# Performance work log

Measured on AMD Instinct MI355X. Metric: run time of the kernel, lower is better.

The kernel has to match this reference:

```python
import jax, jax.numpy as jnp
import numpy as np
from jax import lax

B, C, H, W = 8, 2, 1024, 1024
K = 500            # max_num
POST_MAX = 83      # circle_nms post_max_size
NMS_THRESH = 4.0   # squared-distance threshold in grid units
SCORE_THR = 0.1
# post_center_range converted to grid units per CenterPointBBoxCoder.__init__
PCR_LOW = jnp.array([-100.0, -100.0, -10.0], dtype=jnp.float32)
PCR_HIGH = jnp.array([1124.0, 1124.0, 10.0], dtype=jnp.float32)


def setup_inputs() -> dict:
    key = jax.random.key(0)
    ks = jax.random.split(key, 7)
    return {
        "heat": jax.random.uniform(ks[0], (B, C, H, W), dtype=jnp.float32),
        "reg": jax.random.normal(ks[1], (B, 2, H, W), dtype=jnp.float32),
        "rot_sine": jax.random.normal(ks[2], (B, 1, H, W), dtype=jnp.float32),
        "rot_cosine": jax.random.normal(ks[3], (B, 1, H, W), dtype=jnp.float32),
        "hei": jax.random.normal(ks[4], (B, 1, H, W), dtype=jnp.float32),
        "dim": jax.random.normal(ks[5], (B, 3, H, W), dtype=jnp.float32),
        "vel": jax.random.normal(ks[6], (B, 2, H, W), dtype=jnp.float32),
    }


def _gather_feat(feat_bnc, inds_bk):
    # feat: [B, N, Ch], inds: [B, K] -> [B, K, Ch]
    return jnp.take_along_axis(feat_bnc, inds_bk[:, :, None], axis=1)


def _transpose_and_gather(feat_bchw, inds_bk):
    # [B, Ch, H, W] -> gather at flat HW indices -> [B, K, Ch]
    b, c, h, w = feat_bchw.shape
    f = feat_bchw.transpose(0, 2, 3, 1).reshape(b, h * w, c)
    return _gather_feat(f, inds_bk)


def _topk(scores):
    # scores: [B, C, H, W]
    b, c, h, w = scores.shape
    topk_scores, topk_inds = lax.top_k(scores.reshape(b, c, h * w), K)  # [B,C,K]
    topk_inds = topk_inds % (h * w)
    topk_ys = (topk_inds // w).astype(jnp.float32)
    topk_xs = (topk_inds % w).astype(jnp.float32)
    topk_score, topk_ind = lax.top_k(topk_scores.reshape(b, c * K), K)  # [B,K]
    topk_clses = (topk_ind // K).astype(jnp.int32)
    gather2 = lambda t: jnp.take_along_axis(t.reshape(b, c * K), topk_ind, axis=1)
    return topk_score, gather2(topk_inds), topk_clses, gather2(topk_ys), gather2(topk_xs)


def _circle_nms_keep(x, y, s):
    # Sequential circle NMS per image (jit-compatible fori_loop).
    k = x.shape[0]
    order = jnp.argsort(-s)
    xs, ys = x[order], y[order]
    idx = jnp.arange(k)

    def body(i, supp):
        d2 = (xs - xs[i]) ** 2 + (ys - ys[i]) ** 2
        new = supp | ((idx > i) & (d2 <= NMS_THRESH))
        return jnp.where(supp[i], supp, new)

    supp = lax.fori_loop(0, k, body, jnp.zeros(k, dtype=bool))
    keep_sorted = ~supp
    keep_sorted = keep_sorted & (jnp.cumsum(keep_sorted.astype(jnp.int32)) <= POST_MAX)
    return jnp.zeros(k, dtype=bool).at[order].set(keep_sorted)


def reference(heat, reg, rot_sine, rot_cosine, hei, dim, vel):
    scores, inds, clses, ys, xs = _topk(heat)            # [B,K] each
    reg_g = _transpose_and_gather(reg, inds)             # [B,K,2]
    xs = xs[:, :, None] + reg_g[:, :, 0:1]
    ys = ys[:, :, None] + reg_g[:, :, 1:2]
    rot = jnp.arctan2(_transpose_and_gather(rot_sine, inds),
                      _transpose_and_gather(rot_cosine, inds))  # [B,K,1]
    hei_g = _transpose_and_gather(hei, inds)             # [B,K,1]
    dim_g = _transpose_and_gather(dim, inds)             # [B,K,3]
    vel_g = _transpose_and_gather(vel, inds)             # [B,K,2]
    boxes = jnp.concatenate([xs, ys, hei_g, dim_g, rot, vel_g], axis=2)  # [B,K,9]

    valid = (boxes[..., :3] >= PCR_LOW).all(-1) & (boxes[..., :3] <= PCR_HIGH).all(-1)
    valid = valid & (scores > SCORE_THR)

    nms_scores = jnp.where(valid, scores, -1e9)
    keep = jax.vmap(_circle_nms_keep)(boxes[..., 0], boxes[..., 1], nms_scores) & valid
    return boxes, scores, clses.astype(jnp.float32), valid, keep
```

## Files before the change

kernel.cpp:

```cpp
#include <hip/hip_runtime.h>
#include <stdint.h>

typedef unsigned int u32;
typedef unsigned long long u64;

#define HW (1024*1024)
#define KTOP 500
#define CAP 8192u
#define POST_MAX 83
#define DELTA_THR 9728u

#define WS_CNT2  0
#define WS_CAND  32768
#define WS_SORT  1081344


__global__ __launch_bounds__(256) void k1_collect(const float* __restrict__ heat,
                                                  u32* cnt2, uint2* cand){
  __shared__ uint2 lbuf[64];
  __shared__ u32 lcnt;
  int s     = blockIdx.x >> 7;
  int chunk = blockIdx.x & 127;
  int tid   = threadIdx.x;
  if (tid == 0) lcnt = 0;
  __syncthreads();
  const float4* hp = (const float4*)(heat + (size_t)s*HW + (size_t)chunk*8192);
  float4 v[8];
  #pragma unroll
  for (int i = 0; i < 8; ++i) v[i] = hp[i*256 + tid];
  #pragma unroll
  for (int i = 0; i < 8; ++i){
    u32 idx0 = (u32)chunk*8192u + (u32)(i*256 + tid)*4u;
    float vals[4] = {v[i].x, v[i].y, v[i].z, v[i].w};
    #pragma unroll
    for (int c = 0; c < 4; ++c){
      u32 bits  = __float_as_uint(vals[c]);
      u32 delta = 0x3F800000u - bits;
      if (delta < DELTA_THR){
        u32 p = atomicAdd(&lcnt, 1u);
        if (p < 64u) lbuf[p] = make_uint2(bits, idx0 + (u32)c);
      }
    }
  }
  __syncthreads();
  u32 n = lcnt;
  u32 stored = (n < 64u) ? n : 64u;
  if (tid < stored) cand[(size_t)s*CAP + (u32)chunk*64u + tid] = lbuf[tid];
  if (tid == 0) cnt2[s*128 + chunk] = stored | ((n > 64u) ? 0x80000000u : 0u);
}

__global__ __launch_bounds__(1024) void kR_rank(const float* __restrict__ heat,
                                                const u32* __restrict__ cnt2,
                                                uint2* cand, uint2* sorted){
  __shared__ __align__(16) u64 lkey[CAP];
  __shared__ u32 coff[129];
  __shared__ u32 lhist[256];
  __shared__ u32 lc;
  __shared__ int t2s;
  __shared__ u32 meta;
  int s = blockIdx.x >> 1, h = blockIdx.x & 1, t = threadIdx.x;

  if (t == 0){
    u32 tot = 0, ov = 0;
    for (int c = 0; c < 128; ++c){
      u32 w = cnt2[s*128 + c];
      ov |= (w >> 31);
      coff[c] = tot;
      tot += (w & 0x7FFFFFFFu);
    }
    coff[128] = tot;
    meta = tot | (ov << 31);
  }
  __syncthreads();
  u32 total = meta & 0x7FFFFFFFu;
  bool fb = ((meta >> 31) != 0u) || (total < (u32)KTOP);
  u32 n;

  if (!fb){
    n = total;
    for (u32 i = t; i < CAP; i += 1024){
      u32 c = i >> 6, j = i & 63u;
      u32 cnt_c = coff[c+1] - coff[c];
      if (j < cnt_c){
        uint2 cv = cand[(size_t)s*CAP + i];
        lkey[coff[c] + j] = ((u64)(~cv.x) << 32) | (u64)cv.y;
      }
    }
    __syncthreads();
  } else {
    if (h) return;
    if (t < 256) lhist[t] = 0;
    if (t == 0) lc = 0;
    __syncthreads();
    const float4* hp = (const float4*)(heat + (size_t)s*HW);
    for (int it = 0; it < 256; ++it){
      float4 v = hp[it*1024 + t];
      #pragma unroll
      for (int c = 0; c < 4; ++c){
        float val = (c==0)?v.x:(c==1)?v.y:(c==2)?v.z:v.w;
        u32 bits  = __float_as_uint(val);
        u32 delta = 0x3F800000u - bits;
        u32 bin   = delta >> 16; if (bin > 255u) bin = 255u;
        atomicAdd(&lhist[bin], 1u);
      }
    }
    __syncthreads();
    if (t == 0){
      u32 cum = 0; u32 b1 = 255u;
      for (u32 bb = 0; bb < 256u; ++bb){
        cum += lhist[bb];
        if (cum >= (u32)KTOP){ b1 = bb; break; }
      }
      t2s = (int)(0x3F800000u - ((b1 + 1u) << 16) + 1u);
    }
    __syncthreads();
    int t2 = t2s;
    for (int it = 0; it < 256; ++it){
      float4 v = hp[it*1024 + t];
      u32 idx0 = (u32)(it*1024 + t)*4u;
      #pragma unroll
      for (int c = 0; c < 4; ++c){
        float val = (c==0)?v.x:(c==1)?v.y:(c==2)?v.z:v.w;
        int bits = (int)__float_as_uint(val);
        if (bits >= t2){
          u32 p = atomicAdd(&lc, 1u);
          if (p < CAP) cand[(size_t)s*CAP + p] = make_uint2((u32)bits, idx0 + (u32)c);
        }
      }
    }
    __syncthreads();
    n = (lc < CAP) ? lc : CAP;
    for (u32 i = t; i < n; i += 1024){
      uint2 cv = cand[(size_t)s*CAP + i];
      lkey[i] = ((u64)(~cv.x) << 32) | (u64)cv.y;
    }
    __syncthreads();
  }

  u32 lo = fb ? 0u : (u32)h * ((n + 1u) >> 1);
  u32 hi = fb ? n  : (h ? n : ((n + 1u) >> 1));
  const ulonglong2* lk2 = (const ulonglong2*)lkey;
  u32 np  = n >> 1;
  u32 np8 = np & ~7u;
  for (u32 me = lo + t; me < hi; me += 1024){
    u64 k0 = lkey[me];
    u32 r = 0;
    u32 j = 0;
    for (; j < np8; j += 8){
      ulonglong2 a0 = lk2[j+0];
      ulonglong2 a1 = lk2[j+1];
      ulonglong2 a2 = lk2[j+2];
      ulonglong2 a3 = lk2[j+3];
      ulonglong2 a4 = lk2[j+4];
      ulonglong2 a5 = lk2[j+5];
      ulonglong2 a6 = lk2[j+6];
      ulonglong2 a7 = lk2[j+7];
      r += (a0.x < k0) + (a0.y < k0) + (a1.x < k0) + (a1.y < k0);
      r += (a2.x < k0) + (a2.y < k0) + (a3.x < k0) + (a3.y < k0);
      r += (a4.x < k0) + (a4.y < k0) + (a5.x < k0) + (a5.y < k0);
      r += (a6.x < k0) + (a6.y < k0) + (a7.x < k0) + (a7.y < k0);
    }
    for (; j < np; ++j){
      ulonglong2 kk = lk2[j];
      r += (kk.x < k0) + (kk.y < k0);
    }
    if (n & 1u) r += (lkey[n-1] < k0) ? 1u : 0u;
    if (r < 512u)
      sorted[s*512 + (int)r] = make_uint2(~(u32)(k0 >> 32), (u32)k0);
  }
}

__global__ __launch_bounds__(1024) void kT_tail(const uint2* __restrict__ sorted,
                                                const float* __restrict__ reg,
                                                const float* __restrict__ rots,
                                                const float* __restrict__ rotc,
                                                const float* __restrict__ hei,
                                                const float* __restrict__ dim,
                                                const float* __restrict__ vel,
                                                float* out){
  __shared__ u64 k2a[512], k2b[512];
  __shared__ uint2 fin[512];
  __shared__ float xo[512], yo[512];
  __shared__ float2 pts[512];
  __shared__ int order[512], vld[512];
  __shared__ u32 ordvl[512];
  __shared__ int wsum[16];
  __shared__ u64 keepw[8];
  int b = blockIdx.x, t = threadIdx.x;

  uint2 mye = make_uint2(0u, 0u);
  if (t < 512){
    mye = sorted[(b*2 + 0)*512 + t];
    k2a[t] = ((u64)(~mye.x) << 32) | (u64)t;
  } else {
    int p = t - 512;
    mye = sorted[(b*2 + 1)*512 + p];
    k2b[p] = ((u64)(~mye.x) << 32) | (u64)(KTOP + p);
  }
  if (t < 8) keepw[t] = 0ull;
  __syncthreads();

  if (t < KTOP){
    u64 K = k2a[t];
    int lo = 0, hi = KTOP;
    while (lo < hi){ int mid = (lo + hi) >> 1; if (k2b[mid] < K) lo = mid + 1; else hi = mid; }
    int m = t + lo;
    if (m < KTOP){
      fin[m] = make_uint2(mye.x, mye.y & 0xFFFFFu);
      out[36000 + b*KTOP + m] = __uint_as_float(mye.x);
      out[40000 + b*KTOP + m] = 0.0f;
    }
  } else if (t >= 512 && t < 512 + KTOP){
    int p = t - 512;
    u64 K = k2b[p];
    int lo = 0, hi = KTOP;
    while (lo < hi){ int mid = (lo + hi) >> 1; if (k2a[mid] < K) lo = mid + 1; else hi = mid; }
    int m = p + lo;
    if (m < KTOP){
      fin[m] = make_uint2(mye.x, (mye.y & 0xFFFFFu) | (1u << 20));
      out[36000 + b*KTOP + m] = __uint_as_float(mye.x);
      out[40000 + b*KTOP + m] = 1.0f;
    }
  }
  __syncthreads();

  float x = 0.f, y = 0.f; int v = 0;
  if (t < KTOP){
    uint2 e = fin[t];
    u32 ind = e.y & 0xFFFFFu;
    float mysc = __uint_as_float(e.x);
    float xs0 = (float)(ind & 1023u);
    float ys0 = (float)(ind >> 10);
    size_t bb = (size_t)b;
    float r0  = reg [(bb*2 + 0)*HW + ind];
    float r1  = reg [(bb*2 + 1)*HW + ind];
    float sn  = rots[ bb       *HW + ind];
    float cs  = rotc[ bb       *HW + ind];
    float he  = hei [ bb       *HW + ind];
    float d0  = dim [(bb*3 + 0)*HW + ind];
    float d1  = dim [(bb*3 + 1)*HW + ind];
    float d2v = dim [(bb*3 + 2)*HW + ind];
    float v0  = vel [(bb*2 + 0)*HW + ind];
    float v1  = vel [(bb*2 + 1)*HW + ind];
    x = xs0 + r0; y = ys0 + r1;
    float rot = atan2f(sn, cs);
    float* bx = out + (size_t)(b*KTOP + t)*9;
    bx[0]=x; bx[1]=y; bx[2]=he; bx[3]=d0; bx[4]=d1; bx[5]=d2v; bx[6]=rot; bx[7]=v0; bx[8]=v1;
    v = ((x >= -100.0f) && (x <= 1124.0f) &&
         (y >= -100.0f) && (y <= 1124.0f) &&
         (he >= -10.0f) && (he <= 10.0f) && (mysc > 0.1f)) ? 1 : 0;
    out[44000 + b*KTOP + t] = v ? 1.0f : 0.0f;
  }
  if (t < 512){ xo[t] = x; yo[t] = y; vld[t] = v; }

  u64 bm = __ballot(v != 0);
  int lane = t & 63, wv = t >> 6;
  if (lane == 0) wsum[wv] = __popcll(bm);
  __syncthreads();
  int off = 0, nValid = 0;
  #pragma unroll
  for (int w2 = 0; w2 < 8; ++w2){
    int sv = wsum[w2];
    nValid += sv;
    if (w2 < wv) off += sv;
  }
  int incl = off + __popcll(bm & ((~0ull) >> (63 - lane)));
  if (t < KTOP){
    int excl = incl - v;
    int slot = v ? excl : (nValid + (t - excl));
    order[slot] = t;
  }
  __syncthreads();

  if (t < KTOP){
    int p = order[t];
    pts[t] = make_float2(xo[p], yo[p]);
    ordvl[t] = (u32)p | ((u32)vld[p] << 31);
  } else if (t < 512){
    pts[t] = make_float2(1e30f, 1e30f);
    ordvl[t] = 0u;
  }
  __syncthreads();

  if (t < 64){
    int nv = nValid;
    float kx0 = 1e30f, ky0 = 1e30f, kx1 = 1e30f, ky1 = 1e30f;
    int count = 0;
    u64 curw = 0ull;
    int i = 0;
    float2 pcur = pts[0];
    float2 pnxt = pts[1];
    for (i = 0; i < nv; ++i){
      float2 p = pcur;
      pcur = pnxt;
      pnxt = pts[(i + 2 < 512) ? (i + 2) : 511];
      float dx0 = __fsub_rn(kx0, p.x), dy0 = __fsub_rn(ky0, p.y);
      float dx1 = __fsub_rn(kx1, p.x), dy1 = __fsub_rn(ky1, p.y);
      float d20 = __fadd_rn(__fmul_rn(dx0,dx0), __fmul_rn(dy0,dy0));
      float d21 = __fadd_rn(__fmul_rn(dx1,dx1), __fmul_rn(dy1,dy1));
      bool nearby = (d20 <= 4.0f) || (d21 <= 4.0f);
      if (!__any(nearby)){
        curw |= (1ull << (i & 63));
        if (count < 64){
          if (t == count){ kx0 = p.x; ky0 = p.y; }
        } else {
          if (t == count - 64){ kx1 = p.x; ky1 = p.y; }
        }
        ++count;
        if (count == POST_MAX) break;
      }
      if ((i & 63) == 63){
        if (t == 0) keepw[i >> 6] |= curw;
        curw = 0ull;
      }
    }
    if (t == 0 && curw != 0ull){
      int wi = i >> 6; if (wi > 7) wi = 7;
      keepw[wi] |= curw;
    }
  }
  __syncthreads();

  if (t < KTOP){
    int bit = (int)((keepw[t >> 6] >> (t & 63)) & 1ull);
    u32 pv = ordvl[t];
    int p = (int)(pv & 511u);
    out[48000 + b*KTOP + p] = (bit && (pv >> 31)) ? 1.0f : 0.0f;
  }
}

extern "C" void kernel_launch(void* const* d_in, const int* in_sizes, int n_in,
                              void* d_out, int out_size, void* d_ws, size_t ws_size,
                              hipStream_t stream){
  const float* heat = (const float*)d_in[0];
  const float* reg  = (const float*)d_in[1];
  const float* rots = (const float*)d_in[2];
  const float* rotc = (const float*)d_in[3];
  const float* hei  = (const float*)d_in[4];
  const float* dim  = (const float*)d_in[5];
  const float* vel  = (const float*)d_in[6];
  float* out = (float*)d_out;
  char* ws = (char*)d_ws;
  u32*   cnt2   = (u32*)  (ws + WS_CNT2);
  uint2* cand   = (uint2*)(ws + WS_CAND);
  uint2* sorted = (uint2*)(ws + WS_SORT);

  k1_collect <<<2048, 256, 0, stream>>>(heat, cnt2, cand);
  kR_rank    <<<32,  1024, 0, stream>>>(heat, cnt2, cand, sorted);
  kT_tail    <<<8,   1024, 0, stream>>>(sorted, reg, rots, rotc, hei, dim, vel, out);
}
```

Baseline: 54.12 us.

## Shrink rank and tail kernels to one smaller block per slice

The rank kernel now runs one 512-thread block per batch-class slice instead of two 1024-thread half blocks, so each thread ranks more keys. The tail kernel drops from 1024 to 256 threads and uses strided loops, with a two-element-per-thread ballot prefix scan. The 128 chunk counts are also staged through shared memory before the serial prefix sum. The intent is to cut block launch and barrier cost on these tiny grids, at the price of much less parallelism in the O(n^2) ranking loop and the gather phase.

```diff
diff --git a/kernel.cpp b/kernel.cpp
--- a/kernel.cpp
+++ b/kernel.cpp
@@ -49,21 +49,24 @@
   if (tid == 0) cnt2[s*128 + chunk] = stored | ((n > 64u) ? 0x80000000u : 0u);
 }
 
-__global__ __launch_bounds__(1024) void kR_rank(const float* __restrict__ heat,
-                                                const u32* __restrict__ cnt2,
-                                                uint2* cand, uint2* sorted){
+__global__ __launch_bounds__(512) void kR_rank(const float* __restrict__ heat,
+                                               const u32* __restrict__ cnt2,
+                                               uint2* cand, uint2* sorted){
   __shared__ __align__(16) u64 lkey[CAP];
+  __shared__ u32 tmpc[128];
   __shared__ u32 coff[129];
   __shared__ u32 lhist[256];
   __shared__ u32 lc;
   __shared__ int t2s;
   __shared__ u32 meta;
-  int s = blockIdx.x >> 1, h = blockIdx.x & 1, t = threadIdx.x;
-
+  int s = blockIdx.x, t = threadIdx.x;
+
+  if (t < 128) tmpc[t] = cnt2[s*128 + t];
+  __syncthreads();
   if (t == 0){
     u32 tot = 0, ov = 0;
     for (int c = 0; c < 128; ++c){
-      u32 w = cnt2[s*128 + c];
+      u32 w = tmpc[c];
       ov |= (w >> 31);
       coff[c] = tot;
       tot += (w & 0x7FFFFFFFu);
@@ -78,7 +81,7 @@
 
   if (!fb){
     n = total;
-    for (u32 i = t; i < CAP; i += 1024){
+    for (u32 i = t; i < CAP; i += 512){
       u32 c = i >> 6, j = i & 63u;
       u32 cnt_c = coff[c+1] - coff[c];
       if (j < cnt_c){
@@ -88,13 +91,12 @@
     }
     __syncthreads();
   } else {
-    if (h) return;
     if (t < 256) lhist[t] = 0;
     if (t == 0) lc = 0;
     __syncthreads();
     const float4* hp = (const float4*)(heat + (size_t)s*HW);
-    for (int it = 0; it < 256; ++it){
-      float4 v = hp[it*1024 + t];
+    for (int it = 0; it < 512; ++it){
+      float4 v = hp[it*512 + t];
       #pragma unroll
       for (int c = 0; c < 4; ++c){
         float val = (c==0)?v.x:(c==1)?v.y:(c==2)?v.z:v.w;
@@ -115,9 +117,9 @@
     }
     __syncthreads();
     int t2 = t2s;
-    for (int it = 0; it < 256; ++it){
-      float4 v = hp[it*1024 + t];
-      u32 idx0 = (u32)(it*1024 + t)*4u;
+    for (int it = 0; it < 512; ++it){
+      float4 v = hp[it*512 + t];
+      u32 idx0 = (u32)(it*512 + t)*4u;
       #pragma unroll
       for (int c = 0; c < 4; ++c){
         float val = (c==0)?v.x:(c==1)?v.y:(c==2)?v.z:v.w;
@@ -130,19 +132,17 @@
     }
     __syncthreads();
     n = (lc < CAP) ? lc : CAP;
-    for (u32 i = t; i < n; i += 1024){
+    for (u32 i = t; i < n; i += 512){
       uint2 cv = cand[(size_t)s*CAP + i];
       lkey[i] = ((u64)(~cv.x) << 32) | (u64)cv.y;
     }
     __syncthreads();
   }
 
-  u32 lo = fb ? 0u : (u32)h * ((n + 1u) >> 1);
-  u32 hi = fb ? n  : (h ? n : ((n + 1u) >> 1));
   const ulonglong2* lk2 = (const ulonglong2*)lkey;
   u32 np  = n >> 1;
   u32 np8 = np & ~7u;
-  for (u32 me = lo + t; me < hi; me += 1024){
+  for (u32 me = t; me < n; me += 512){
     u64 k0 = lkey[me];
     u32 r = 0;
     u32 j = 0;
@@ -170,115 +170,125 @@
   }
 }
 
-__global__ __launch_bounds__(1024) void kT_tail(const uint2* __restrict__ sorted,
-                                                const float* __restrict__ reg,
-                                                const float* __restrict__ rots,
-                                                const float* __restrict__ rotc,
-                                                const float* __restrict__ hei,
-                                                const float* __restrict__ dim,
-                                                const float* __restrict__ vel,
-                                                float* out){
+__global__ __launch_bounds__(256) void kT_tail(const uint2* __restrict__ sorted,
+                                               const float* __restrict__ reg,
+                                               const float* __restrict__ rots,
+                                               const float* __restrict__ rotc,
+                                               const float* __restrict__ hei,
+                                               const float* __restrict__ dim,
+                                               const float* __restrict__ vel,
+                                               float* out){
   __shared__ u64 k2a[512], k2b[512];
+  __shared__ uint2 sA[512], sB[512];
   __shared__ uint2 fin[512];
   __shared__ float xo[512], yo[512];
   __shared__ float2 pts[512];
   __shared__ int order[512], vld[512];
   __shared__ u32 ordvl[512];
-  __shared__ int wsum[16];
+  __shared__ int wsum[4];
   __shared__ u64 keepw[8];
   int b = blockIdx.x, t = threadIdx.x;
 
-  uint2 mye = make_uint2(0u, 0u);
-  if (t < 512){
-    mye = sorted[(b*2 + 0)*512 + t];
-    k2a[t] = ((u64)(~mye.x) << 32) | (u64)t;
-  } else {
-    int p = t - 512;
-    mye = sorted[(b*2 + 1)*512 + p];
-    k2b[p] = ((u64)(~mye.x) << 32) | (u64)(KTOP + p);
+  for (int i = t; i < 512; i += 256){
+    uint2 e0 = sorted[(b*2 + 0)*512 + i];
+    uint2 e1 = sorted[(b*2 + 1)*512 + i];
+    sA[i] = e0; sB[i] = e1;
+    k2a[i] = ((u64)(~e0.x) << 32) | (u64)i;
+    k2b[i] = ((u64)(~e1.x) << 32) | (u64)(KTOP + i);
   }
   if (t < 8) keepw[t] = 0ull;
   __syncthreads();
 
-  if (t < KTOP){
-    u64 K = k2a[t];
-    int lo = 0, hi = KTOP;
-    while (lo < hi){ int mid = (lo + hi) >> 1; if (k2b[mid] < K) lo = mid + 1; else hi = mid; }
-    int m = t + lo;
-    if (m < KTOP){
-      fin[m] = make_uint2(mye.x, mye.y & 0xFFFFFu);
-      out[36000 + b*KTOP + m] = __uint_as_float(mye.x);
-      out[40000 + b*KTOP + m] = 0.0f;
-    }
-  } else if (t >= 512 && t < 512 + KTOP){
-    int p = t - 512;
-    u64 K = k2b[p];
-    int lo = 0, hi = KTOP;
-    while (lo < hi){ int mid = (lo + hi) >> 1; if (k2a[mid] < K) lo = mid + 1; else hi = mid; }
-    int m = p + lo;
-    if (m < KTOP){
-      fin[m] = make_uint2(mye.x, (mye.y & 0xFFFFFu) | (1u << 20));
-      out[36000 + b*KTOP + m] = __uint_as_float(mye.x);
-      out[40000 + b*KTOP + m] = 1.0f;
-    }
-  }
-  __syncthreads();
-
-  float x = 0.f, y = 0.f; int v = 0;
-  if (t < KTOP){
-    uint2 e = fin[t];
-    u32 ind = e.y & 0xFFFFFu;
-    float mysc = __uint_as_float(e.x);
-    float xs0 = (float)(ind & 1023u);
-    float ys0 = (float)(ind >> 10);
-    size_t bb = (size_t)b;
-    float r0  = reg [(bb*2 + 0)*HW + ind];
-    float r1  = reg [(bb*2 + 1)*HW + ind];
-    float sn  = rots[ bb       *HW + ind];
-    float cs  = rotc[ bb       *HW + ind];
-    float he  = hei [ bb       *HW + ind];
-    float d0  = dim [(bb*3 + 0)*HW + ind];
-    float d1  = dim [(bb*3 + 1)*HW + ind];
-    float d2v = dim [(bb*3 + 2)*HW + ind];
-    float v0  = vel [(bb*2 + 0)*HW + ind];
-    float v1  = vel [(bb*2 + 1)*HW + ind];
-    x = xs0 + r0; y = ys0 + r1;
-    float rot = atan2f(sn, cs);
-    float* bx = out + (size_t)(b*KTOP + t)*9;
-    bx[0]=x; bx[1]=y; bx[2]=he; bx[3]=d0; bx[4]=d1; bx[5]=d2v; bx[6]=rot; bx[7]=v0; bx[8]=v1;
-    v = ((x >= -100.0f) && (x <= 1124.0f) &&
-         (y >= -100.0f) && (y <= 1124.0f) &&
-         (he >= -10.0f) && (he <= 10.0f) && (mysc > 0.1f)) ? 1 : 0;
-    out[44000 + b*KTOP + t] = v ? 1.0f : 0.0f;
-  }
-  if (t < 512){ xo[t] = x; yo[t] = y; vld[t] = v; }
-
-  u64 bm = __ballot(v != 0);
+  for (int i = t; i < KTOP; i += 256){
+    {
+      u64 K = k2a[i];
+      int lo = 0, hi = KTOP;
+      while (lo < hi){ int mid = (lo + hi) >> 1; if (k2b[mid] < K) lo = mid + 1; else hi = mid; }
+      int m = i + lo;
+      if (m < KTOP){
+        uint2 e = sA[i];
+        fin[m] = make_uint2(e.x, e.y & 0xFFFFFu);
+        out[36000 + b*KTOP + m] = __uint_as_float(e.x);
+        out[40000 + b*KTOP + m] = 0.0f;
+      }
+    }
+    {
+      u64 K = k2b[i];
+      int lo = 0, hi = KTOP;
+      while (lo < hi){ int mid = (lo + hi) >> 1; if (k2a[mid] < K) lo = mid + 1; else hi = mid; }
+      int m = i + lo;
+      if (m < KTOP){
+        uint2 e = sB[i];
+        fin[m] = make_uint2(e.x, (e.y & 0xFFFFFu) | (1u << 20));
+        out[36000 + b*KTOP + m] = __uint_as_float(e.x);
+        out[40000 + b*KTOP + m] = 1.0f;
+      }
+    }
+  }
+  __syncthreads();
+
+  for (int i = t; i < 512; i += 256){
+    float x = 0.f, y = 0.f; int v = 0;
+    if (i < KTOP){
+      uint2 e = fin[i];
+      u32 ind = e.y & 0xFFFFFu;
+      float mysc = __uint_as_float(e.x);
+      float xs0 = (float)(ind & 1023u);
+      float ys0 = (float)(ind >> 10);
+      size_t bb = (size_t)b;
+      float r0  = reg [(bb*2 + 0)*HW + ind];
+      float r1  = reg [(bb*2 + 1)*HW + ind];
+      float sn  = rots[ bb       *HW + ind];
+      float cs  = rotc[ bb       *HW + ind];
+      float he  = hei [ bb       *HW + ind];
+      float d0  = dim [(bb*3 + 0)*HW + ind];
+      float d1  = dim [(bb*3 + 1)*HW + ind];
+      float d2v = dim [(bb*3 + 2)*HW + ind];
+      float v0  = vel [(bb*2 + 0)*HW + ind];
+      float v1  = vel [(bb*2 + 1)*HW + ind];
+      x = xs0 + r0; y = ys0 + r1;
+      float rot = atan2f(sn, cs);
+      float* bx = out + (size_t)(b*KTOP + i)*9;
+      bx[0]=x; bx[1]=y; bx[2]=he; bx[3]=d0; bx[4]=d1; bx[5]=d2v; bx[6]=rot; bx[7]=v0; bx[8]=v1;
+      v = ((x >= -100.0f) && (x <= 1124.0f) &&
+           (y >= -100.0f) && (y <= 1124.0f) &&
+           (he >= -10.0f) && (he <= 10.0f) && (mysc > 0.1f)) ? 1 : 0;
+      out[44000 + b*KTOP + i] = v ? 1.0f : 0.0f;
+    }
+    xo[i] = x; yo[i] = y; vld[i] = v;
+  }
+  __syncthreads();
+
+  int e0 = 2*t, e1 = 2*t + 1;
+  int v0 = vld[e0], v1 = vld[e1];
+  u64 b0 = __ballot(v0 != 0);
+  u64 b1 = __ballot(v1 != 0);
   int lane = t & 63, wv = t >> 6;
-  if (lane == 0) wsum[wv] = __popcll(bm);
+  if (lane == 0) wsum[wv] = __popcll(b0) + __popcll(b1);
   __syncthreads();
   int off = 0, nValid = 0;
   #pragma unroll
-  for (int w2 = 0; w2 < 8; ++w2){
+  for (int w2 = 0; w2 < 4; ++w2){
     int sv = wsum[w2];
     nValid += sv;
     if (w2 < wv) off += sv;
   }
-  int incl = off + __popcll(bm & ((~0ull) >> (63 - lane)));
-  if (t < KTOP){
-    int excl = incl - v;
-    int slot = v ? excl : (nValid + (t - excl));
-    order[slot] = t;
-  }
-  __syncthreads();
-
-  if (t < KTOP){
-    int p = order[t];
-    pts[t] = make_float2(xo[p], yo[p]);
-    ordvl[t] = (u32)p | ((u32)vld[p] << 31);
-  } else if (t < 512){
-    pts[t] = make_float2(1e30f, 1e30f);
-    ordvl[t] = 0u;
+  u64 LT = (lane == 0) ? 0ull : ((~0ull) >> (64 - lane));
+  int exA = off + __popcll(b0 & LT) + __popcll(b1 & LT);
+  int exB = exA + v0;
+  if (e0 < KTOP){ int slot = v0 ? exA : (nValid + (e0 - exA)); order[slot] = e0; }
+  if (e1 < KTOP){ int slot = v1 ? exB : (nValid + (e1 - exB)); order[slot] = e1; }
+  __syncthreads();
+
+  for (int i = t; i < 512; i += 256){
+    if (i < KTOP){
+      int p = order[i];
+      pts[i] = make_float2(xo[p], yo[p]);
+      ordvl[i] = (u32)p | ((u32)vld[p] << 31);
+    } else {
+      pts[i] = make_float2(1e30f, 1e30f);
+      ordvl[i] = 0u;
+    }
   }
   __syncthreads();
 
@@ -321,9 +331,9 @@
   }
   __syncthreads();
 
-  if (t < KTOP){
-    int bit = (int)((keepw[t >> 6] >> (t & 63)) & 1ull);
-    u32 pv = ordvl[t];
+  for (int e = t; e < KTOP; e += 256){
+    int bit = (int)((keepw[e >> 6] >> (e & 63)) & 1ull);
+    u32 pv = ordvl[e];
     int p = (int)(pv & 511u);
     out[48000 + b*KTOP + p] = (bit && (pv >> 31)) ? 1.0f : 0.0f;
   }
@@ -346,6 +356,6 @@
   uint2* sorted = (uint2*)(ws + WS_SORT);
 
   k1_collect <<<2048, 256, 0, stream>>>(heat, cnt2, cand);
-  kR_rank    <<<32,  1024, 0, stream>>>(heat, cnt2, cand, sorted);
-  kT_tail    <<<8,   1024, 0, stream>>>(sorted, reg, rots, rotc, hei, dim, vel, out);
+  kR_rank    <<<16,   512, 0, stream>>>(heat, cnt2, cand, sorted);
+  kT_tail    <<<8,    256, 0, stream>>>(sorted, reg, rots, rotc, hei, dim, vel, out);
 }
```

Result: slower. 62.50 us (+15.5%).
